# Optimization experiments

Hardware: AMD Instinct MI355X
Metric: run time of the kernel (lower is better)

Reference implementation:

```python
import jax, jax.numpy as jnp
import numpy as np

B, N, C, E = 512, 128, 4, 300   # batch, context events, components per event, embed dim
V = 50000                       # event-arg vocab (padding row appended -> V+1)
H1, H2 = 512, 256               # arg_composition_layer_sizes
NF = 8                          # num_extracted_features
K = 11                          # KNRM kernel count

MUS = jnp.array([1.0, 0.9, 0.7, 0.5, 0.3, 0.1, -0.1, -0.3, -0.5, -0.7, -0.9], dtype=jnp.float32)
SIGMAS = jnp.array([1e-3] + [0.1] * 10, dtype=jnp.float32)


def setup_inputs() -> dict:
    key = jax.random.key(0)
    ks = jax.random.split(key, 16)
    s = 0.05
    inp = {
        "event_table": jax.random.normal(ks[0], (V + 1, E), jnp.float32) * s,
        "W1": jax.random.normal(ks[1], (H1, C * E), jnp.float32) * s,
        "b1": jnp.zeros((H1,), jnp.float32),
        "W2": jax.random.normal(ks[2], (H2, H1), jnp.float32) * s,
        "b2": jnp.zeros((H2,), jnp.float32),
        "Wv": jax.random.normal(ks[3], (9, E), jnp.float32) * s,
        "bv": jnp.zeros((9,), jnp.float32),
        "Wc": jax.random.normal(ks[4], (1, NF + 9 + K), jnp.float32) * s,
        "bc": jnp.zeros((1,), jnp.float32),
        "batch_event": jax.random.randint(ks[5], (B, C), 0, V),
        "batch_features": jax.random.normal(ks[6], (B, NF), jnp.float32),
        "batch_distances": jax.random.uniform(ks[7], (B, 9), jnp.float32),
        "batch_context": jax.random.randint(ks[8], (B, N, C), 0, V),
        "batch_slots": jax.random.randint(ks[9], (B,), 0, C),
    }
    return inp


def _mlp(x, W1, b1, W2, b2):
    x = jax.nn.relu(x @ W1.T + b1)
    return jax.nn.relu(x @ W2.T + b2)


def _l2norm(x):
    n = jnp.linalg.norm(x, axis=-1, keepdims=True)
    return x / jnp.maximum(n, 1e-12)


def _kernel_pool(trans):
    # trans: [B, M, N] cosine similarities; RBF kernels over values, reduce N.
    k = jnp.exp(-(trans[..., None] - MUS) ** 2 / (2.0 * SIGMAS ** 2))  # [B,M,N,K]
    pooled = jnp.sum(k, axis=2)                                        # [B,M,K]
    return jnp.log(jnp.clip(pooled, 1e-10, None)) * 0.01


def reference(event_table, W1, b1, W2, b2, Wv, bv, Wc, bc,
              batch_event, batch_features, batch_distances, batch_context, batch_slots):
    # embedding lookups
    event_emb = event_table[batch_event]        # [B, C, E]
    context_emb = event_table[batch_context]    # [B, N, C, E]

    # distance encoding: event-dependent Gaussian kernels (predicate detached)
    predicates = jax.lax.stop_gradient(event_emb[:, 1, :])       # [B, E]
    variances = jax.nn.softplus(predicates @ Wv.T + bv)          # [B, 9]
    dist_emb = jnp.exp(-(batch_distances * batch_distances) / variances)
    extracted = jnp.concatenate([dist_emb, batch_features], axis=1)  # [B, 17]

    # event / context representations via shared arg-composition MLP
    event_repr = _mlp(event_emb.reshape(B, 1, C * E), W1, b1, W2, b2)      # [B,1,H2]
    context_repr = _mlp(context_emb.reshape(B, N, C * E), W1, b1, W2, b2)  # [B,N,H2]

    # cosine-similarity bmm + kernel pooling
    trans = jnp.einsum('bmd,bnd->bmn', _l2norm(event_repr), _l2norm(context_repr))  # [B,1,N]
    kp_mtx = _kernel_pool(trans)                                                    # [B,1,K]

    all_features = jnp.concatenate([extracted[:, None, :], kp_mtx], axis=-1)  # [B,1,17+K]
    scores = (all_features @ Wc.T + bc)[..., 0]                               # [B,1]
    return jax.nn.sigmoid(scores)
```

## Files before the change

kernel.cpp:

```cpp
#include <hip/hip_runtime.h>
#include <hip/hip_bf16.h>

#define B_    512
#define N_    128
#define E_    300
#define EP    304
#define CE    1200
#define KP1   1216
#define H1_   512
#define H2_   256
#define MT    66048
#define VP1   50001
#define NTT   (VP1 * 38)
#define NTW1  (H1_ * 152)
#define NTW2  (H2_ * H1_ / 8)

typedef __attribute__((ext_vector_type(8))) short bf16x8;
typedef __attribute__((ext_vector_type(4))) float f32x4;
typedef __attribute__((ext_vector_type(4))) unsigned short us4;
typedef __attribute__((ext_vector_type(8))) unsigned short us8;

static __device__ __forceinline__ unsigned short f2bf(float f) {
  unsigned int u = __float_as_uint(f);
  u += 0x7fffu + ((u >> 16) & 1u);
  return (unsigned short)(u >> 16);
}
static __device__ __forceinline__ float bf2f(unsigned short h) {
  return __uint_as_float(((unsigned int)h) << 16);
}
static __device__ __forceinline__ void gl16(const void* g, void* l) {
  __builtin_amdgcn_global_load_lds((const __attribute__((address_space(1))) unsigned int*)g,
                                   (__attribute__((address_space(3))) unsigned int*)l, 16, 0, 0);
}
static __device__ __forceinline__ unsigned long long pk8f8(
    float f0, float f1, float f2, float f3, float f4, float f5, float f6, float f7) {
  int lo = __builtin_amdgcn_cvt_pk_fp8_f32(f0, f1, 0, false);
  lo = __builtin_amdgcn_cvt_pk_fp8_f32(f2, f3, lo, true);
  int hi = __builtin_amdgcn_cvt_pk_fp8_f32(f4, f5, 0, false);
  hi = __builtin_amdgcn_cvt_pk_fp8_f32(f6, f7, hi, true);
  return ((unsigned long long)(unsigned int)hi << 32) | (unsigned int)lo;
}

__global__ __launch_bounds__(256) void convert_k(
    const float* __restrict__ table, const float* __restrict__ W1, const float* __restrict__ W2,
    unsigned char* __restrict__ tb8, unsigned char* __restrict__ W1f8,
    unsigned short* __restrict__ W2b) {
  int i = blockIdx.x * 256 + threadIdx.x;
  if (i < NTT) {
    int r = i / 38, ch = i - r * 38;
    int e = ch * 8;
    unsigned long long o;
    if (e < 296) {
      float4 a = *reinterpret_cast<const float4*>(table + (size_t)r * 300 + e);
      float4 b = *reinterpret_cast<const float4*>(table + (size_t)r * 300 + e + 4);
      o = pk8f8(a.x, a.y, a.z, a.w, b.x, b.y, b.z, b.w);
    } else {
      float4 a = *reinterpret_cast<const float4*>(table + (size_t)r * 300 + 296);
      o = pk8f8(a.x, a.y, a.z, a.w, 0.f, 0.f, 0.f, 0.f);
    }
    *reinterpret_cast<unsigned long long*>(tb8 + (size_t)r * EP + e) = o;
  } else if (i < NTT + NTW1) {
    int j = i - NTT;
    int r = j / 152, ch = j - r * 152;
    int k = ch * 8;
    int c = (k >= 912) ? 3 : (k >= 608) ? 2 : (k >= 304) ? 1 : 0;
    int e = k - c * EP;
    const float* src = W1 + (size_t)r * CE + c * 300 + e;
    unsigned long long o;
    if (e < 296) {
      float4 a = *reinterpret_cast<const float4*>(src);
      float4 b = *reinterpret_cast<const float4*>(src + 4);
      o = pk8f8(a.x, a.y, a.z, a.w, b.x, b.y, b.z, b.w);
    } else {
      float4 a = *reinterpret_cast<const float4*>(src);
      o = pk8f8(a.x, a.y, a.z, a.w, 0.f, 0.f, 0.f, 0.f);
    }
    *reinterpret_cast<unsigned long long*>(W1f8 + (size_t)r * KP1 + k) = o;
  } else if (i < NTT + NTW1 + NTW2) {
    int j = i - NTT - NTW1;
    float4 a = *reinterpret_cast<const float4*>(W2 + (size_t)j * 8);
    float4 b = *reinterpret_cast<const float4*>(W2 + (size_t)j * 8 + 4);
    us8 o;
    o[0]=f2bf(a.x); o[1]=f2bf(a.y); o[2]=f2bf(a.z); o[3]=f2bf(a.w);
    o[4]=f2bf(b.x); o[5]=f2bf(b.y); o[6]=f2bf(b.z); o[7]=f2bf(b.w);
    *reinterpret_cast<us8*>(W2b + (size_t)j * 8) = o;
  }
}

__global__ __launch_bounds__(256) void gemm1_k(
    const unsigned char* __restrict__ tb8, const unsigned char* __restrict__ W1f8,
    const float* __restrict__ b1, const int* __restrict__ bev, const int* __restrict__ bctx,
    unsigned short* __restrict__ H1buf) {
  __shared__ unsigned char As[3][128 * 64];
  __shared__ unsigned char Bs[3][128 * 64];

  const int tid  = threadIdx.x;
  const int lane = tid & 63;
  const int w    = tid >> 6;
  const int wr   = w >> 1, wc = w & 1;
  const int wgid = (blockIdx.x & 7) * 258 + (blockIdx.x >> 3);
  const int m0 = (wgid >> 2) * 128;
  const int n0 = (wgid & 3) * 128;
  const int fr = lane & 15, fg = lane >> 4;

  const int l16  = (tid & 3) ^ ((tid >> 3) & 3);
  const int aoff = l16 * 16;
  int idx[2][4];
#pragma unroll
  for (int i = 0; i < 2; ++i) {
    int mrow = m0 + i * 64 + (tid >> 2);
    int bidx = mrow / 129, nidx = mrow - bidx * 129;
    const int* p = (nidx < 128) ? bctx + ((size_t)bidx * 128 + nidx) * 4
                                : bev + (size_t)bidx * 4;
#pragma unroll
    for (int c = 0; c < 4; ++c) idx[i][c] = p[c];
  }
  const unsigned char* bsrc0 = W1f8 + (size_t)(n0 + (tid >> 2)) * KP1 + aoff;
  const unsigned char* bsrc1 = bsrc0 + (size_t)64 * KP1;

  const int s_r  = (fr >> 1) & 3;
  const int qo0  = (((fg >> 1) ^ s_r) * 16) + (fg & 1) * 8;
  const int qo1  = (((2 + (fg >> 1)) ^ s_r) * 16) + (fg & 1) * 8;

  f32x4 acc[4][4];
#pragma unroll
  for (int mi = 0; mi < 4; ++mi)
#pragma unroll
    for (int ni = 0; ni < 4; ++ni)
#pragma unroll
      for (int r = 0; r < 4; ++r) acc[mi][ni][r] = 0.f;

#define STAGE1(BUF, KT)                                                       \
  do {                                                                        \
    int k_ = (KT) * 64 + aoff;                                                \
    int c_ = (k_ >= 912) ? 3 : (k_ >= 608) ? 2 : (k_ >= 304) ? 1 : 0;         \
    int e_ = k_ - c_ * EP;                                                    \
    int id0 = (c_ == 0) ? idx[0][0] : (c_ == 1) ? idx[0][1]                   \
            : (c_ == 2) ? idx[0][2] : idx[0][3];                              \
    int id1 = (c_ == 0) ? idx[1][0] : (c_ == 1) ? idx[1][1]                   \
            : (c_ == 2) ? idx[1][2] : idx[1][3];                              \
    gl16(tb8 + (size_t)id0 * EP + e_, &As[BUF][w * 1024]);                    \
    gl16(tb8 + (size_t)id1 * EP + e_, &As[BUF][4096 + w * 1024]);             \
    gl16(bsrc0 + (size_t)(KT) * 64, &Bs[BUF][w * 1024]);                      \
    gl16(bsrc1 + (size_t)(KT) * 64, &Bs[BUF][4096 + w * 1024]);               \
  } while (0)

#define COMPUTE1(BUF)                                                         \
  do {                                                                        \
    long af0[4], af1[4], bf0[4], bf1[4];                                      \
    _Pragma("unroll")                                                         \
    for (int mi = 0; mi < 4; ++mi) {                                          \
      int rb = (wr * 64 + mi * 16 + fr) * 64;                                 \
      af0[mi] = *reinterpret_cast<const long*>(&As[BUF][rb + qo0]);           \
      af1[mi] = *reinterpret_cast<const long*>(&As[BUF][rb + qo1]);           \
    }                                                                         \
    _Pragma("unroll")                                                         \
    for (int ni = 0; ni < 4; ++ni) {                                          \
      int rb = (wc * 64 + ni * 16 + fr) * 64;                                 \
      bf0[ni] = *reinterpret_cast<const long*>(&Bs[BUF][rb + qo0]);           \
      bf1[ni] = *reinterpret_cast<const long*>(&Bs[BUF][rb + qo1]);           \
    }                                                                         \
    __builtin_amdgcn_s_setprio(1);                                            \
    _Pragma("unroll")                                                         \
    for (int mi = 0; mi < 4; ++mi)                                            \
      _Pragma("unroll")                                                       \
      for (int ni = 0; ni < 4; ++ni)                                          \
        acc[mi][ni] = __builtin_amdgcn_mfma_f32_16x16x32_fp8_fp8(             \
            af0[mi], bf0[ni], acc[mi][ni], 0, 0, 0);                          \
    _Pragma("unroll")                                                         \
    for (int mi = 0; mi < 4; ++mi)                                            \
      _Pragma("unroll")                                                       \
      for (int ni = 0; ni < 4; ++ni)                                          \
        acc[mi][ni] = __builtin_amdgcn_mfma_f32_16x16x32_fp8_fp8(             \
            af1[mi], bf1[ni], acc[mi][ni], 0, 0, 0);                          \
    __builtin_amdgcn_s_setprio(0);                                            \
  } while (0)

  STAGE1(0, 0);
  STAGE1(1, 1);
  int cur = 0, nx = 2;
  for (int t = 0; t < 18; ++t) {
    asm volatile("s_waitcnt vmcnt(4)" ::: "memory");
    __builtin_amdgcn_s_barrier();
    if (t + 2 < 19) STAGE1(nx, t + 2);
    COMPUTE1(cur);
    cur = (cur == 2) ? 0 : cur + 1;
    nx  = (nx  == 2) ? 0 : nx  + 1;
  }
  asm volatile("s_waitcnt vmcnt(0)" ::: "memory");
  __builtin_amdgcn_s_barrier();
  COMPUTE1(cur);
#undef STAGE1
#undef COMPUTE1

  float bb[4];
#pragma unroll
  for (int ni = 0; ni < 4; ++ni) bb[ni] = b1[n0 + wc * 64 + ni * 16 + fr];
#pragma unroll
  for (int mi = 0; mi < 4; ++mi)
#pragma unroll
    for (int ni = 0; ni < 4; ++ni)
#pragma unroll
      for (int r = 0; r < 4; ++r) {
        float v = fmaxf(acc[mi][ni][r] + bb[ni], 0.f);
        int row = m0 + wr * 64 + mi * 16 + fg * 4 + r;
        int col = n0 + wc * 64 + ni * 16 + fr;
        H1buf[(size_t)row * H1_ + col] = f2bf(v);
      }
}

__global__ __launch_bounds__(512) void gemm2_k(
    const unsigned short* __restrict__ H1buf, const unsigned short* __restrict__ W2b,
    const float* __restrict__ b2, unsigned short* __restrict__ RPR) {
  __shared__ unsigned short As[3][128 * 32];
  __shared__ unsigned short Bs[3][256 * 32];
  __shared__ float rpart[128][4];
  __shared__ float rinv[128];

  const int tid  = threadIdx.x;
  const int lane = tid & 63;
  const int w    = tid >> 6;
  const int wr   = w >> 2, wc = w & 3;
  const int m0   = blockIdx.x * 128;
  const int fr = lane & 15, fg = lane >> 4;

  const int l16 = (tid & 3) ^ ((tid >> 3) & 3);
  const unsigned short* asrc = H1buf + (size_t)(m0 + (tid >> 2)) * H1_ + l16 * 8;
  const unsigned short* bsrc = W2b + (size_t)(tid >> 2) * H1_ + l16 * 8;
  const int p16f = fg ^ ((fr >> 1) & 3);

  f32x4 acc[4][4];
#pragma unroll
  for (int mi = 0; mi < 4; ++mi)
#pragma unroll
    for (int ni = 0; ni < 4; ++ni)
#pragma unroll
      for (int r = 0; r < 4; ++r) acc[mi][ni][r] = 0.f;

#define STAGE2(BUF, KT)                                                       \
  do {                                                                        \
    gl16(asrc + (KT) * 32, &As[BUF][w * 512]);                                \
    gl16(bsrc + (KT) * 32, &Bs[BUF][w * 512]);                                \
    gl16(bsrc + 128 * H1_ + (KT) * 32, &Bs[BUF][4096 + w * 512]);             \
  } while (0)

#define COMPUTE2(BUF)                                                         \
  do {                                                                        \
    bf16x8 af[4], bfv[4];                                                     \
    _Pragma("unroll")                                                         \
    for (int mi = 0; mi < 4; ++mi)                                            \
      af[mi] = *reinterpret_cast<const bf16x8*>(                              \
          &As[BUF][(wr * 64 + mi * 16 + fr) * 32 + p16f * 8]);                \
    _Pragma("unroll")                                                         \
    for (int ni = 0; ni < 4; ++ni)                                            \
      bfv[ni] = *reinterpret_cast<const bf16x8*>(                             \
          &Bs[BUF][(wc * 64 + ni * 16 + fr) * 32 + p16f * 8]);                \
    __builtin_amdgcn_s_setprio(1);                                            \
    _Pragma("unroll")                                                         \
    for (int mi = 0; mi < 4; ++mi)                                            \
      _Pragma("unroll")                                                       \
      for (int ni = 0; ni < 4; ++ni)                                          \
        acc[mi][ni] = __builtin_amdgcn_mfma_f32_16x16x32_bf16(                \
            af[mi], bfv[ni], acc[mi][ni], 0, 0, 0);                           \
    __builtin_amdgcn_s_setprio(0);                                            \
  } while (0)

  STAGE2(0, 0);
  STAGE2(1, 1);
  int cur = 0, nx = 2;
  for (int t = 0; t < 15; ++t) {
    asm volatile("s_waitcnt vmcnt(3)" ::: "memory");
    __builtin_amdgcn_s_barrier();
    if (t + 2 < 16) STAGE2(nx, t + 2);
    COMPUTE2(cur);
    cur = (cur == 2) ? 0 : cur + 1;
    nx  = (nx  == 2) ? 0 : nx  + 1;
  }
  asm volatile("s_waitcnt vmcnt(0)" ::: "memory");
  __builtin_amdgcn_s_barrier();
  COMPUTE2(cur);
#undef STAGE2
#undef COMPUTE2

  float bb[4];
#pragma unroll
  for (int ni = 0; ni < 4; ++ni) bb[ni] = b2[wc * 64 + ni * 16 + fr];
#pragma unroll
  for (int mi = 0; mi < 4; ++mi)
#pragma unroll
    for (int ni = 0; ni < 4; ++ni)
#pragma unroll
      for (int r = 0; r < 4; ++r)
        acc[mi][ni][r] = fmaxf(acc[mi][ni][r] + bb[ni], 0.f);

#pragma unroll
  for (int mi = 0; mi < 4; ++mi)
#pragma unroll
    for (int r = 0; r < 4; ++r) {
      float s = 0.f;
#pragma unroll
      for (int ni = 0; ni < 4; ++ni) s += acc[mi][ni][r] * acc[mi][ni][r];
      s += __shfl_xor(s, 1); s += __shfl_xor(s, 2);
      s += __shfl_xor(s, 4); s += __shfl_xor(s, 8);
      if (fr == 0) rpart[wr * 64 + mi * 16 + fg * 4 + r][wc] = s;
    }
  __syncthreads();
  if (tid < 128) {
    float s = rpart[tid][0] + rpart[tid][1] + rpart[tid][2] + rpart[tid][3];
    rinv[tid] = 1.f / fmaxf(sqrtf(s), 1e-12f);
  }
  __syncthreads();

#pragma unroll
  for (int mi = 0; mi < 4; ++mi)
#pragma unroll
    for (int r = 0; r < 4; ++r) {
      int lrow = wr * 64 + mi * 16 + fg * 4 + r;
      float sc = rinv[lrow];
#pragma unroll
      for (int ni = 0; ni < 4; ++ni) {
        int col = wc * 64 + ni * 16 + fr;
        RPR[(size_t)(m0 + lrow) * H2_ + col] = f2bf(acc[mi][ni][r] * sc);
      }
    }
}

__global__ __launch_bounds__(256) void final_k(
    const float* __restrict__ table, const float* __restrict__ Wv, const float* __restrict__ bv,
    const float* __restrict__ Wc, const float* __restrict__ bc, const int* __restrict__ bev,
    const float* __restrict__ bdist, const float* __restrict__ bfeat,
    const unsigned short* __restrict__ RPR, float* __restrict__ out) {
  const int b = blockIdx.x, tid = threadIdx.x, lane = tid & 63, w = tid >> 6;
  __shared__ float pred[E_];
  __shared__ float tarr[128];
  __shared__ float var_s[9];
  __shared__ float pool_s[2][11];

  const float MU[11]  = {1.0f, 0.9f, 0.7f, 0.5f, 0.3f, 0.1f, -0.1f, -0.3f, -0.5f, -0.7f, -0.9f};
  const float IS2[11] = {500000.f, 50.f, 50.f, 50.f, 50.f, 50.f, 50.f, 50.f, 50.f, 50.f, 50.f};

  const int prow = bev[b * 4 + 1];
  for (int e = tid; e < E_; e += 256) pred[e] = table[(size_t)prow * E_ + e];
  __syncthreads();

  if (tid < 144) {
    int j = tid >> 4, l = tid & 15;
    float s = 0.f;
    for (int e = l; e < E_; e += 16) s += pred[e] * Wv[j * E_ + e];
    s += __shfl_xor(s, 1); s += __shfl_xor(s, 2);
    s += __shfl_xor(s, 4); s += __shfl_xor(s, 8);
    if (l == 0) {
      float x = s + bv[j];
      var_s[j] = fmaxf(x, 0.f) + log1pf(expf(-fabsf(x)));
    }
  }

  const unsigned short* evp = RPR + ((size_t)b * 129 + 128) * H2_;
  us4 e4 = *reinterpret_cast<const us4*>(evp + lane * 4);
  const float e0 = bf2f(e4[0]), e1 = bf2f(e4[1]), e2 = bf2f(e4[2]), e3 = bf2f(e4[3]);
  for (int k = 0; k < 32; ++k) {
    int n = w * 32 + k;
    const unsigned short* cp = RPR + ((size_t)b * 129 + n) * H2_;
    us4 c4 = *reinterpret_cast<const us4*>(cp + lane * 4);
    float d = e0 * bf2f(c4[0]) + e1 * bf2f(c4[1]) + e2 * bf2f(c4[2]) + e3 * bf2f(c4[3]);
#pragma unroll
    for (int off = 32; off; off >>= 1) d += __shfl_xor(d, off);
    if (lane == 0) tarr[n] = d;
  }
  __syncthreads();

  if (tid < 128) {
    float t = tarr[tid];
    float kv[11];
#pragma unroll
    for (int kk = 0; kk < 11; ++kk) {
      float u = t - MU[kk];
      kv[kk] = expf(-u * u * IS2[kk]);
    }
#pragma unroll
    for (int off = 32; off; off >>= 1)
#pragma unroll
      for (int kk = 0; kk < 11; ++kk) kv[kk] += __shfl_xor(kv[kk], off);
    if (lane == 0)
#pragma unroll
      for (int kk = 0; kk < 11; ++kk) pool_s[w][kk] = kv[kk];
  }
  __syncthreads();

  if (tid == 0) {
    float score = bc[0];
    for (int j = 0; j < 9; ++j) {
      float d = bdist[b * 9 + j];
      score += Wc[j] * expf(-(d * d) / var_s[j]);
    }
    for (int i = 0; i < 8; ++i) score += Wc[9 + i] * bfeat[b * 8 + i];
    for (int kk = 0; kk < 11; ++kk) {
      float p = fmaxf(pool_s[0][kk] + pool_s[1][kk], 1e-10f);
      score += Wc[17 + kk] * (0.01f * logf(p));
    }
    out[b] = 1.f / (1.f + expf(-score));
  }
}

extern "C" void kernel_launch(void* const* d_in, const int* in_sizes, int n_in,
                              void* d_out, int out_size, void* d_ws, size_t ws_size,
                              hipStream_t stream) {
  const float* table = (const float*)d_in[0];
  const float* W1    = (const float*)d_in[1];
  const float* b1    = (const float*)d_in[2];
  const float* W2    = (const float*)d_in[3];
  const float* b2    = (const float*)d_in[4];
  const float* Wv    = (const float*)d_in[5];
  const float* bv    = (const float*)d_in[6];
  const float* Wc    = (const float*)d_in[7];
  const float* bc    = (const float*)d_in[8];
  const int*   bev   = (const int*)d_in[9];
  const float* bfeat = (const float*)d_in[10];
  const float* bdist = (const float*)d_in[11];
  const int*   bctx  = (const int*)d_in[12];
  float* out = (float*)d_out;

  auto align64 = [](size_t x) { return (x + 63) & ~(size_t)63; };
  size_t off = 0;
  size_t o_tb8  = off; off += align64((size_t)VP1 * EP);
  size_t o_W1f8 = off; off += align64((size_t)H1_ * KP1);
  size_t o_W2b  = off; off += align64((size_t)H2_ * H1_ * 2);
  size_t o_H1   = off; off += align64((size_t)MT * H1_ * 2);
  size_t o_RPR  = off; off += align64((size_t)MT * H2_ * 2);
  if (ws_size < off) {
    hipMemsetAsync(d_out, 0xBF, (size_t)out_size * 4, stream);
    return;
  }
  char* ws = (char*)d_ws;
  unsigned char*  tb8   = (unsigned char*)(ws + o_tb8);
  unsigned char*  W1f8  = (unsigned char*)(ws + o_W1f8);
  unsigned short* W2b   = (unsigned short*)(ws + o_W2b);
  unsigned short* H1buf = (unsigned short*)(ws + o_H1);
  unsigned short* RPR   = (unsigned short*)(ws + o_RPR);

  const int conv_items = NTT + NTW1 + NTW2;
  hipLaunchKernelGGL(convert_k, dim3((conv_items + 255) / 256), dim3(256), 0, stream,
                     table, W1, W2, tb8, W1f8, W2b);
  hipLaunchKernelGGL(gemm1_k, dim3(MT / 128 * 4), dim3(256), 0, stream,
                     tb8, W1f8, b1, bev, bctx, H1buf);
  hipLaunchKernelGGL(gemm2_k, dim3(MT / 128), dim3(512), 0, stream, H1buf, W2b, b2, RPR);
  hipLaunchKernelGGL(final_k, dim3(B_), dim3(256), 0, stream,
                     table, Wv, bv, Wc, bc, bev, bdist, bfeat, RPR, out);
}
```

Before: 165.3 us.

## Permute fp8 K layout so each lane loads 16 bytes per LDS fragment

Pads each embedding component to 320 bytes (5 full 64-byte K tiles per component) and pre-permutes the fp8 table and W1 within each 64-byte chunk. This lets each lane fetch both MFMA k-halves with a single 16-byte LDS read instead of two 8-byte reads, and simplifies the component/offset arithmetic in staging. In exchange the K loop grows from 19 to 20 tiles with extra zero padding, and the converted table gets larger.

```diff
diff --git a/kernel.cpp b/kernel.cpp
--- a/kernel.cpp
+++ b/kernel.cpp
@@ -4,21 +4,22 @@
 #define B_    512
 #define N_    128
 #define E_    300
-#define EP    304
+#define EP    320
 #define CE    1200
-#define KP1   1216
+#define KP1   1280
 #define H1_   512
 #define H2_   256
 #define MT    66048
 #define VP1   50001
-#define NTT   (VP1 * 38)
-#define NTW1  (H1_ * 152)
+#define NTT   (VP1 * 40)
+#define NTW1  (H1_ * 160)
 #define NTW2  (H2_ * H1_ / 8)
 
 typedef __attribute__((ext_vector_type(8))) short bf16x8;
 typedef __attribute__((ext_vector_type(4))) float f32x4;
 typedef __attribute__((ext_vector_type(4))) unsigned short us4;
 typedef __attribute__((ext_vector_type(8))) unsigned short us8;
+typedef __attribute__((ext_vector_type(2))) long lx2;
 
 static __device__ __forceinline__ unsigned short f2bf(float f) {
   unsigned int u = __float_as_uint(f);
@@ -41,41 +42,38 @@
   return ((unsigned long long)(unsigned int)hi << 32) | (unsigned int)lo;
 }
 
+static __device__ __forceinline__ unsigned long long pack_unit(const float* __restrict__ comp,
+                                                               int e) {
+  if (e < 296) {
+    float4 a = *reinterpret_cast<const float4*>(comp + e);
+    float4 b = *reinterpret_cast<const float4*>(comp + e + 4);
+    return pk8f8(a.x, a.y, a.z, a.w, b.x, b.y, b.z, b.w);
+  } else if (e == 296) {
+    float4 a = *reinterpret_cast<const float4*>(comp + 296);
+    return pk8f8(a.x, a.y, a.z, a.w, 0.f, 0.f, 0.f, 0.f);
+  }
+  return 0ULL;
+}
+
 __global__ __launch_bounds__(256) void convert_k(
     const float* __restrict__ table, const float* __restrict__ W1, const float* __restrict__ W2,
     unsigned char* __restrict__ tb8, unsigned char* __restrict__ W1f8,
     unsigned short* __restrict__ W2b) {
   int i = blockIdx.x * 256 + threadIdx.x;
   if (i < NTT) {
-    int r = i / 38, ch = i - r * 38;
-    int e = ch * 8;
-    unsigned long long o;
-    if (e < 296) {
-      float4 a = *reinterpret_cast<const float4*>(table + (size_t)r * 300 + e);
-      float4 b = *reinterpret_cast<const float4*>(table + (size_t)r * 300 + e + 4);
-      o = pk8f8(a.x, a.y, a.z, a.w, b.x, b.y, b.z, b.w);
-    } else {
-      float4 a = *reinterpret_cast<const float4*>(table + (size_t)r * 300 + 296);
-      o = pk8f8(a.x, a.y, a.z, a.w, 0.f, 0.f, 0.f, 0.f);
-    }
-    *reinterpret_cast<unsigned long long*>(tb8 + (size_t)r * EP + e) = o;
+    int r = i / 40, j = i - r * 40;
+    int s = j >> 3, p = j & 7;
+    int e = s * 64 + ((p & 1) * 4 + (p >> 1)) * 8;
+    unsigned long long o = pack_unit(table + (size_t)r * 300, e);
+    *reinterpret_cast<unsigned long long*>(tb8 + (size_t)r * EP + j * 8) = o;
   } else if (i < NTT + NTW1) {
     int j = i - NTT;
-    int r = j / 152, ch = j - r * 152;
-    int k = ch * 8;
-    int c = (k >= 912) ? 3 : (k >= 608) ? 2 : (k >= 304) ? 1 : 0;
-    int e = k - c * EP;
-    const float* src = W1 + (size_t)r * CE + c * 300 + e;
-    unsigned long long o;
-    if (e < 296) {
-      float4 a = *reinterpret_cast<const float4*>(src);
-      float4 b = *reinterpret_cast<const float4*>(src + 4);
-      o = pk8f8(a.x, a.y, a.z, a.w, b.x, b.y, b.z, b.w);
-    } else {
-      float4 a = *reinterpret_cast<const float4*>(src);
-      o = pk8f8(a.x, a.y, a.z, a.w, 0.f, 0.f, 0.f, 0.f);
-    }
-    *reinterpret_cast<unsigned long long*>(W1f8 + (size_t)r * KP1 + k) = o;
+    int r = j / 160, jj = j - r * 160;
+    int t = jj >> 3, p = jj & 7;
+    int k = t * 64 + ((p & 1) * 4 + (p >> 1)) * 8;
+    int c = k / EP, e = k - c * EP;
+    unsigned long long o = pack_unit(W1 + (size_t)r * CE + c * 300, e);
+    *reinterpret_cast<unsigned long long*>(W1f8 + (size_t)r * KP1 + jj * 8) = o;
   } else if (i < NTT + NTW1 + NTW2) {
     int j = i - NTT - NTW1;
     float4 a = *reinterpret_cast<const float4*>(W2 + (size_t)j * 8);
@@ -103,8 +101,7 @@
   const int n0 = (wgid & 3) * 128;
   const int fr = lane & 15, fg = lane >> 4;
 
-  const int l16  = (tid & 3) ^ ((tid >> 3) & 3);
-  const int aoff = l16 * 16;
+  const int l16 = (tid & 3) ^ ((tid >> 3) & 3);
   int idx[2][4];
 #pragma unroll
   for (int i = 0; i < 2; ++i) {
@@ -115,12 +112,9 @@
 #pragma unroll
     for (int c = 0; c < 4; ++c) idx[i][c] = p[c];
   }
-  const unsigned char* bsrc0 = W1f8 + (size_t)(n0 + (tid >> 2)) * KP1 + aoff;
+  const unsigned char* bsrc0 = W1f8 + (size_t)(n0 + (tid >> 2)) * KP1 + l16 * 16;
   const unsigned char* bsrc1 = bsrc0 + (size_t)64 * KP1;
-
-  const int s_r  = (fr >> 1) & 3;
-  const int qo0  = (((fg >> 1) ^ s_r) * 16) + (fg & 1) * 8;
-  const int qo1  = (((2 + (fg >> 1)) ^ s_r) * 16) + (fg & 1) * 8;
+  const int p16f = fg ^ ((fr >> 1) & 3);
 
   f32x4 acc[4][4];
 #pragma unroll
@@ -132,9 +126,8 @@
 
 #define STAGE1(BUF, KT)                                                       \
   do {                                                                        \
-    int k_ = (KT) * 64 + aoff;                                                \
-    int c_ = (k_ >= 912) ? 3 : (k_ >= 608) ? 2 : (k_ >= 304) ? 1 : 0;         \
-    int e_ = k_ - c_ * EP;                                                    \
+    int c_ = (KT) / 5;                                                        \
+    int e_ = ((KT) - c_ * 5) * 64 + l16 * 16;                                 \
     int id0 = (c_ == 0) ? idx[0][0] : (c_ == 1) ? idx[0][1]                   \
             : (c_ == 2) ? idx[0][2] : idx[0][3];                              \
     int id1 = (c_ == 0) ? idx[1][0] : (c_ == 1) ? idx[1][1]                   \
@@ -147,42 +140,38 @@
 
 #define COMPUTE1(BUF)                                                         \
   do {                                                                        \
-    long af0[4], af1[4], bf0[4], bf1[4];                                      \
-    _Pragma("unroll")                                                         \
-    for (int mi = 0; mi < 4; ++mi) {                                          \
-      int rb = (wr * 64 + mi * 16 + fr) * 64;                                 \
-      af0[mi] = *reinterpret_cast<const long*>(&As[BUF][rb + qo0]);           \
-      af1[mi] = *reinterpret_cast<const long*>(&As[BUF][rb + qo1]);           \
-    }                                                                         \
-    _Pragma("unroll")                                                         \
-    for (int ni = 0; ni < 4; ++ni) {                                          \
-      int rb = (wc * 64 + ni * 16 + fr) * 64;                                 \
-      bf0[ni] = *reinterpret_cast<const long*>(&Bs[BUF][rb + qo0]);           \
-      bf1[ni] = *reinterpret_cast<const long*>(&Bs[BUF][rb + qo1]);           \
-    }                                                                         \
+    lx2 af[4], bf[4];                                                         \
+    _Pragma("unroll")                                                         \
+    for (int mi = 0; mi < 4; ++mi)                                            \
+      af[mi] = *reinterpret_cast<const lx2*>(                                 \
+          &As[BUF][(wr * 64 + mi * 16 + fr) * 64 + p16f * 16]);               \
+    _Pragma("unroll")                                                         \
+    for (int ni = 0; ni < 4; ++ni)                                            \
+      bf[ni] = *reinterpret_cast<const lx2*>(                                 \
+          &Bs[BUF][(wc * 64 + ni * 16 + fr) * 64 + p16f * 16]);               \
     __builtin_amdgcn_s_setprio(1);                                            \
     _Pragma("unroll")                                                         \
     for (int mi = 0; mi < 4; ++mi)                                            \
       _Pragma("unroll")                                                       \
       for (int ni = 0; ni < 4; ++ni)                                          \
         acc[mi][ni] = __builtin_amdgcn_mfma_f32_16x16x32_fp8_fp8(             \
-            af0[mi], bf0[ni], acc[mi][ni], 0, 0, 0);                          \
+            af[mi][0], bf[ni][0], acc[mi][ni], 0, 0, 0);                      \
     _Pragma("unroll")                                                         \
     for (int mi = 0; mi < 4; ++mi)                                            \
       _Pragma("unroll")                                                       \
       for (int ni = 0; ni < 4; ++ni)                                          \
         acc[mi][ni] = __builtin_amdgcn_mfma_f32_16x16x32_fp8_fp8(             \
-            af1[mi], bf1[ni], acc[mi][ni], 0, 0, 0);                          \
+            af[mi][1], bf[ni][1], acc[mi][ni], 0, 0, 0);                      \
     __builtin_amdgcn_s_setprio(0);                                            \
   } while (0)
 
   STAGE1(0, 0);
   STAGE1(1, 1);
   int cur = 0, nx = 2;
-  for (int t = 0; t < 18; ++t) {
+  for (int t = 0; t < 19; ++t) {
     asm volatile("s_waitcnt vmcnt(4)" ::: "memory");
     __builtin_amdgcn_s_barrier();
-    if (t + 2 < 19) STAGE1(nx, t + 2);
+    if (t + 2 < 20) STAGE1(nx, t + 2);
     COMPUTE1(cur);
     cur = (cur == 2) ? 0 : cur + 1;
     nx  = (nx  == 2) ? 0 : nx  + 1;
```

After: 154.1 us. 1.07x faster.
